# Performance work log

Measured on AMD Instinct MI355X. Metric: run time of the kernel, lower is better.

Reference implementation:

```python
import jax, jax.numpy as jnp
import numpy as np

H, VS, VT, S, T = 512, 32000, 32000, 256, 256
EPS = 1e-12


def _normalize(x):
    # torch.nn.functional.normalize over last dim, p=2, eps=1e-12
    n = jnp.sqrt(jnp.sum(x * x, axis=-1, keepdims=True))
    return x / jnp.maximum(n, EPS)


def setup_inputs() -> dict:
    key = jax.random.key(0)
    ks = jax.random.split(key, 16)
    std = 0.01
    return {
        'src_nums': jax.random.randint(ks[0], (S,), 0, VS, dtype=jnp.int32),
        'tgt_nums': jax.random.randint(ks[1], (T,), 0, VT, dtype=jnp.int32),
        'enc_emb_W': std * jax.random.normal(ks[2], (VS, H), jnp.float32),
        'enc_h0': std * jax.random.normal(ks[3], (H,), jnp.float32),
        'enc_W_hi': std * jax.random.normal(ks[4], (H, H), jnp.float32),
        'enc_W_hh': std * jax.random.normal(ks[5], (H, H), jnp.float32),
        'enc_b': std * jax.random.normal(ks[6], (H,), jnp.float32),
        'dec_emb_W': std * jax.random.normal(ks[7], (VT, H), jnp.float32),
        'dec_h0': std * jax.random.normal(ks[8], (H,), jnp.float32),
        'dec_W_hi': std * jax.random.normal(ks[9], (H, H), jnp.float32),
        'dec_W_hh': std * jax.random.normal(ks[10], (H, H), jnp.float32),
        'dec_b': std * jax.random.normal(ks[11], (H,), jnp.float32),
        'tnh_W': std * jax.random.normal(ks[12], (H, 2 * H), jnp.float32),
        'tnh_b': std * jax.random.normal(ks[13], (H,), jnp.float32),
        'out_W': std * jax.random.normal(ks[14], (VT, H), jnp.float32),
    }


def reference(src_nums, tgt_nums, enc_emb_W, enc_h0, enc_W_hi, enc_W_hh, enc_b,
              dec_emb_W, dec_h0, dec_W_hi, dec_W_hh, dec_b, tnh_W, tnh_b, out_W):
    # ---- Encoder: embed + normalize, then sequential RNN ----
    src_emb = _normalize(enc_emb_W[src_nums])  # [S, H]

    def enc_step(h, e):
        h2 = jnp.tanh(enc_W_hi @ e + enc_W_hh @ h + enc_b)
        return h2, h2

    _, hs = jax.lax.scan(enc_step, enc_h0, src_emb)
    h_seq = jnp.concatenate([enc_h0[None, :], hs], axis=0)  # [S+1, H]

    # ---- Decoder: per-step attention + output + teacher-forced input ----
    def dec_step(h, t):
        # Bahdanau-style dot attention over encoder states
        weights = jax.nn.softmax(h_seq @ h)        # [S+1]
        c = weights @ h_seq                         # [H]
        z = jnp.tanh(tnh_W @ jnp.concatenate([c, h]) + tnh_b)  # [H]
        logp = jax.nn.log_softmax(out_W @ z)        # [VT]
        nll = -logp[t]
        e = _normalize(dec_emb_W[t])                # [H]
        h2 = jnp.tanh(dec_W_hi @ e + dec_W_hh @ h + dec_b)
        return h2, nll

    _, nlls = jax.lax.scan(dec_step, dec_h0, tgt_nums)
    return jnp.mean(nlls)
```

## Files before the change

kernel.cpp:

```cpp
#include <hip/hip_runtime.h>

typedef _Float16 f16;
typedef _Float16 f16x2 __attribute__((ext_vector_type(2)));
typedef _Float16 half8 __attribute__((ext_vector_type(8)));
typedef float f32x4 __attribute__((ext_vector_type(4)));

#define Hh 512
#define TT 256
#define VTOT 32000
#define S4H 100.0f
#define NO_ELEMS 16384000L
#define NT_ELEMS 524288L

__device__ inline int dot8i4(int a, int b, int c) {
#if __has_builtin(__builtin_amdgcn_sdot8)
    return __builtin_amdgcn_sdot8(a, b, c, false);
#else
    int s = c;
#pragma unroll
    for (int i = 0; i < 8; ++i)
        s += ((a << (28 - 4 * i)) >> 28) * ((b << (28 - 4 * i)) >> 28);
    return s;
#endif
}

__device__ inline float tanh_fast(float x) {
    float ax = fabsf(x);
    float t = __expf(-2.f * ax);
    float th = (1.f - t) * __builtin_amdgcn_rcpf(1.f + t);
    return copysignf(th, x);
}

__device__ inline float block_sum(float v, float* red) {
#pragma unroll
    for (int o = 1; o < 64; o <<= 1) v += __shfl_xor(v, o);
    if ((threadIdx.x & 63) == 0) red[threadIdx.x >> 6] = v;
    __syncthreads();
    v = red[0] + red[1] + red[2] + red[3];
    __syncthreads();
    return v;
}

__device__ inline float block_max(float v, float* red) {
#pragma unroll
    for (int o = 1; o < 64; o <<= 1) v = fmaxf(v, __shfl_xor(v, o));
    if ((threadIdx.x & 63) == 0) red[threadIdx.x >> 6] = v;
    __syncthreads();
    v = fmaxf(fmaxf(red[0], red[1]), fmaxf(red[2], red[3]));
    __syncthreads();
    return v;
}

__global__ void __launch_bounds__(256) k_front(
    const int* __restrict__ src, const int* __restrict__ tgt,
    const float* __restrict__ encW, const float* __restrict__ decW,
    const float* __restrict__ eh0, const float* __restrict__ dh0,
    const float* __restrict__ encWhh, const float* __restrict__ decWhh,
    const float* __restrict__ eWhi, const float* __restrict__ eb,
    const float* __restrict__ dWhi, const float* __restrict__ db,
    float* __restrict__ P, float* __restrict__ h_seq, float* __restrict__ Hd,
    unsigned int* __restrict__ Wq, float* __restrict__ sWf,
    float* __restrict__ denom, float* __restrict__ ltgt) {
    const int b = blockIdx.x, tid = threadIdx.x;
    if (b >= 272) {
        const int c = b - 272;
        float2 v = ((const float2*)(c ? dh0 : eh0))[tid];
        if (c == 0) {
            ((float2*)h_seq)[tid] = v;
#pragma unroll
            for (int k = 0; k < 8; ++k) denom[k * 256 + tid] = 0.f;
        } else {
            ((float2*)Hd)[tid] = v;
            ltgt[tid] = 0.f;
        }
        return;
    }
    if (b >= 16) {
        const int bc = b - 16;
        const int R = bc * 4 + (tid >> 6);
        const int c = R >> 9, r = R & 511, j = tid & 63;
        const float* s = (c ? decWhh : encWhh) + (size_t)r * Hh + j * 8;
        float4 v0 = ((const float4*)s)[0];
        float4 v1 = ((const float4*)s)[1];
        float vv[8] = {v0.x, v0.y, v0.z, v0.w, v1.x, v1.y, v1.z, v1.w};
        float m = 0.f;
#pragma unroll
        for (int k = 0; k < 8; ++k) m = fmaxf(m, fabsf(vv[k]));
#pragma unroll
        for (int o = 1; o < 64; o <<= 1) m = fmaxf(m, __shfl_xor(m, o));
        m = fmaxf(m, 1e-30f);
        float qs = 7.f / m;
        unsigned int dw = 0;
#pragma unroll
        for (int k = 0; k < 8; ++k) {
            int q = (int)rintf(vv[k] * qs);
            dw |= ((unsigned int)(q & 0xF)) << (4 * k);
        }
        const int u = j >> 2, dwi = j & 3;
        Wq[((((size_t)(c * 16 + u)) * 512 + r) << 2) + dwi] = dw;
        if (j == 0) sWf[c * 512 + r] = m * (1.f / (7.f * S4H));
        return;
    }
    const int c = b >> 3;
    const int v0 = (b & 7) * 64;
    const float* Wv = c ? dWhi : eWhi;
    const float* bias = c ? db : eb;
    const float* Etab = c ? decW : encW;
    const int w = tid >> 6, l = tid & 63;
    const int l15 = l & 15, l4 = l >> 4;
    __shared__ __align__(16) f16 Wt[64][136];
    __shared__ __align__(16) f16 Zt[256][136];
    __shared__ float norms[256];
    __shared__ int idxs[256];
    idxs[tid] = c ? tgt[tid] : src[tid];
    __syncthreads();
    {
        const float4* er = (const float4*)(Etab + (size_t)idxs[tid] * Hh);
        float s = 0.f;
        for (int j = 0; j < Hh / 4; ++j) {
            float4 v = er[j];
            s += v.x * v.x + v.y * v.y + v.z * v.z + v.w * v.w;
        }
        norms[tid] = 1.f / fmaxf(sqrtf(s), 1e-12f);
    }
    __syncthreads();

    f32x4 acc[16];
#pragma unroll
    for (int tt = 0; tt < 16; ++tt) acc[tt] = (f32x4){0.f, 0.f, 0.f, 0.f};

    for (int kc = 0; kc < 4; ++kc) {
        const int k0 = kc * 128;
#pragma unroll
        for (int p = 0; p < 8; ++p) {
            int g = p * 256 + tid;
            int row = g >> 5, f4 = g & 31;
            float4 v = *((const float4*)(Wv + (size_t)(v0 + row) * Hh + k0 + f4 * 4));
            f16x2 lo = {(f16)v.x, (f16)v.y};
            f16x2 hi = {(f16)v.z, (f16)v.w};
            uint2 u;
            u.x = __builtin_bit_cast(unsigned, lo);
            u.y = __builtin_bit_cast(unsigned, hi);
            *((uint2*)&Wt[row][f4 * 4]) = u;
        }
#pragma unroll
        for (int p = 0; p < 16; ++p) {
            int g = p * 256 + tid;
            int row = g >> 4, u = g & 15;
            const float* rs = Etab + (size_t)idxs[row] * Hh + k0 + u * 8;
            float4 a0 = ((const float4*)rs)[0];
            float4 a1 = ((const float4*)rs)[1];
            float nm = norms[row];
            f16x2 p0 = {(f16)(a0.x * nm), (f16)(a0.y * nm)};
            f16x2 p1 = {(f16)(a0.z * nm), (f16)(a0.w * nm)};
            f16x2 p2 = {(f16)(a1.x * nm), (f16)(a1.y * nm)};
            f16x2 p3 = {(f16)(a1.z * nm), (f16)(a1.w * nm)};
            uint4 uu;
            uu.x = __builtin_bit_cast(unsigned, p0);
            uu.y = __builtin_bit_cast(unsigned, p1);
            uu.z = __builtin_bit_cast(unsigned, p2);
            uu.w = __builtin_bit_cast(unsigned, p3);
            *((uint4*)&Zt[row][u * 8]) = uu;
        }
        __syncthreads();
        half8 a[4];
#pragma unroll
        for (int ks = 0; ks < 4; ++ks)
            a[ks] = *((const half8*)&Wt[w * 16 + l15][ks * 32 + l4 * 8]);
#pragma unroll
        for (int tt = 0; tt < 16; ++tt) {
#pragma unroll
            for (int ks = 0; ks < 4; ++ks) {
                half8 bb = *((const half8*)&Zt[tt * 16 + l15][ks * 32 + l4 * 8]);
                acc[tt] = __builtin_amdgcn_mfma_f32_16x16x32_f16(a[ks], bb, acc[tt],
                                                                 0, 0, 0);
            }
        }
        __syncthreads();
    }
    const int ibase = v0 + w * 16 + l4 * 4;
    float b0 = bias[ibase], b1 = bias[ibase + 1];
    float b2 = bias[ibase + 2], b3 = bias[ibase + 3];
#pragma unroll
    for (int tt = 0; tt < 16; ++tt) {
        int t = tt * 16 + l15;
        float4 st;
        st.x = acc[tt][0] + b0;
        st.y = acc[tt][1] + b1;
        st.z = acc[tt][2] + b2;
        st.w = acc[tt][3] + b3;
        *((float4*)(P + ((size_t)c * TT + t) * Hh + ibase)) = st;
    }
}

__global__ void __launch_bounds__(512, 2) k_chain(
    const uint4* __restrict__ Wq, const float* __restrict__ sWf,
    const float* __restrict__ P, const float* __restrict__ eh0,
    const float* __restrict__ dh0, float* __restrict__ h_seq,
    float* __restrict__ Hd, const float* __restrict__ outW,
    const float* __restrict__ tnhW, f16* __restrict__ outWh,
    f16* __restrict__ tnhWh) {
    const int c = blockIdx.x, t = threadIdx.x;
    if (c >= 2) {
        const long nthreads = (long)(gridDim.x - 2) * 512;
        long g = (long)(c - 2) * 512 + t;
        const long N8 = (NO_ELEMS + NT_ELEMS) / 8;
        for (; g < N8; g += nthreads) {
            long e = g * 8;
            const float* s;
            f16* d;
            if (e < NO_ELEMS) {
                s = outW + e;
                d = outWh + e;
            } else {
                s = tnhW + (e - NO_ELEMS);
                d = tnhWh + (e - NO_ELEMS);
            }
            float4 v0 = ((const float4*)s)[0];
            float4 v1 = ((const float4*)s)[1];
            f16x2 p0 = {(f16)v0.x, (f16)v0.y};
            f16x2 p1 = {(f16)v0.z, (f16)v0.w};
            f16x2 p2 = {(f16)v1.x, (f16)v1.y};
            f16x2 p3 = {(f16)v1.z, (f16)v1.w};
            uint4 u;
            u.x = __builtin_bit_cast(unsigned, p0);
            u.y = __builtin_bit_cast(unsigned, p1);
            u.z = __builtin_bit_cast(unsigned, p2);
            u.w = __builtin_bit_cast(unsigned, p3);
            *((uint4*)d) = u;
        }
        return;
    }
    __shared__ __align__(16) int hq[2][64];

    uint4 wq[16];
#pragma unroll
    for (int u = 0; u < 16; ++u) wq[u] = Wq[(size_t)(c * 16 + u) * 512 + t];
#pragma unroll
    for (int u = 0; u < 16; ++u)
        asm volatile("" : "+v"(wq[u].x), "+v"(wq[u].y), "+v"(wq[u].z),
                          "+v"(wq[u].w));
    const float frow = sWf[c * 512 + t];

    {
        float hv = (c ? dh0 : eh0)[t];
        int q = (int)rintf(fminf(fmaxf(hv * S4H, -7.f), 7.f));
        int b1 = (q & 0xF) | ((__shfl_down(q, 1) & 0xF) << 4);
        int b2 = (b1 & 0xFF) | ((__shfl_down(b1, 2) & 0xFF) << 8);
        int b4 = (b2 & 0xFFFF) | (__shfl_down(b2, 4) << 16);
        if ((t & 7) == 0) hq[0][t >> 3] = b4;
    }
    __syncthreads();

    const float* Pc = P + (size_t)c * TT * Hh;
    float pv = Pc[t];

    for (int step = 0; step < 256; ++step) {
        float pvn;
        if (step < 255) pvn = Pc[(size_t)(step + 1) * Hh + t];
        const uint4* hp = (const uint4*)hq[step & 1];
        int a0 = 0, a1 = 0;
#pragma unroll
        for (int u = 0; u < 16; ++u) {
            uint4 hv = hp[u];
            uint4 w0 = wq[u];
            a0 = dot8i4((int)w0.x, (int)hv.x, a0);
            a1 = dot8i4((int)w0.y, (int)hv.y, a1);
            a0 = dot8i4((int)w0.z, (int)hv.z, a0);
            a1 = dot8i4((int)w0.w, (int)hv.w, a1);
        }
        float hnew = tanh_fast((float)(a0 + a1) * frow + pv);
        pv = pvn;
        if (c == 0)
            h_seq[(size_t)(step + 1) * Hh + t] = hnew;
        else if (step < 255)
            Hd[(size_t)(step + 1) * Hh + t] = hnew;
        int q = (int)rintf(fminf(fmaxf(hnew * S4H, -7.f), 7.f));
        int b1 = (q & 0xF) | ((__shfl_down(q, 1) & 0xF) << 4);
        int b2 = (b1 & 0xFF) | ((__shfl_down(b1, 2) & 0xFF) << 8);
        int b4 = (b2 & 0xFFFF) | (__shfl_down(b2, 4) << 16);
        if ((t & 7) == 0) hq[(step + 1) & 1][t >> 3] = b4;
        asm volatile("s_waitcnt lgkmcnt(0)\ns_barrier" ::: "memory");
    }
}

__global__ void __launch_bounds__(256) k_scores(const float* __restrict__ h_seq,
                                                const float* __restrict__ Hd,
                                                f16* __restrict__ CHh) {
    const int t0 = blockIdx.x * 4, tid = threadIdx.x;
    __shared__ float hs[4][Hh];
    __shared__ float wts[4][260];
    __shared__ float red[4];
#pragma unroll
    for (int q = 0; q < 4; ++q)
        ((float2*)hs[q])[tid] = ((const float2*)(Hd + (size_t)(t0 + q) * Hh))[tid];
    __syncthreads();
    float a[4] = {0.f, 0.f, 0.f, 0.f};
    {
        const float4* row = (const float4*)(h_seq + (size_t)tid * Hh);
        for (int j = 0; j < Hh / 4; ++j) {
            float4 v = row[j];
#pragma unroll
            for (int q = 0; q < 4; ++q) {
                a[q] += v.x * hs[q][4 * j] + v.y * hs[q][4 * j + 1] +
                        v.z * hs[q][4 * j + 2] + v.w * hs[q][4 * j + 3];
            }
        }
    }
    float sb[4] = {-3.0e38f, -3.0e38f, -3.0e38f, -3.0e38f};
    if (tid == 0) {
        const float4* row = (const float4*)(h_seq + (size_t)256 * Hh);
        float x[4] = {0.f, 0.f, 0.f, 0.f};
        for (int j = 0; j < Hh / 4; ++j) {
            float4 v = row[j];
#pragma unroll
            for (int q = 0; q < 4; ++q) {
                x[q] += v.x * hs[q][4 * j] + v.y * hs[q][4 * j + 1] +
                        v.z * hs[q][4 * j + 2] + v.w * hs[q][4 * j + 3];
            }
        }
#pragma unroll
        for (int q = 0; q < 4; ++q) sb[q] = x[q];
    }
#pragma unroll
    for (int q = 0; q < 4; ++q) {
        float m = block_max(fmaxf(a[q], sb[q]), red);
        float e = expf(a[q] - m);
        float ee = (tid == 0) ? expf(sb[q] - m) : 0.f;
        float tot = block_sum(e + ee, red);
        float inv = 1.f / tot;
        wts[q][tid] = e * inv;
        if (tid == 0) wts[q][256] = ee * inv;
    }
    __syncthreads();
    const float2* hs2 = (const float2*)h_seq;
    float2 cc[4];
#pragma unroll
    for (int q = 0; q < 4; ++q) cc[q] = (float2){0.f, 0.f};
    for (int s = 0; s < 257; ++s) {
        float2 v = hs2[(size_t)s * 256 + tid];
#pragma unroll
        for (int q = 0; q < 4; ++q) {
            float W = wts[q][s];
            cc[q].x += W * v.x;
            cc[q].y += W * v.y;
        }
    }
#pragma unroll
    for (int q = 0; q < 4; ++q) {
        f16* ch = CHh + (size_t)(t0 + q) * (2 * Hh);
        f16x2 o = {(f16)cc[q].x, (f16)cc[q].y};
        ((f16x2*)ch)[tid] = o;
        float2 hh = ((float2*)hs[q])[tid];
        f16x2 ho = {(f16)hh.x, (f16)hh.y};
        ((f16x2*)(ch + Hh))[tid] = ho;
    }
}

template <bool W16>
__global__ void __launch_bounds__(256) k_zmfma(const f16* __restrict__ CHh,
                                               const float* __restrict__ tnhW,
                                               const f16* __restrict__ tnhWh,
                                               const float* __restrict__ tnhb,
                                               f16* __restrict__ Zh) {
    const int v0 = blockIdx.x * 64, t0 = blockIdx.y * 128, tid = threadIdx.x;
    const int w = tid >> 6, l = tid & 63;
    const int l15 = l & 15, l4 = l >> 4;
    __shared__ __align__(16) f16 Wt[64][136];
    __shared__ __align__(16) f16 Zt[128][136];

    f32x4 acc[8];
#pragma unroll
    for (int tt = 0; tt < 8; ++tt) acc[tt] = (f32x4){0.f, 0.f, 0.f, 0.f};

    for (int kc = 0; kc < 8; ++kc) {
        const int k0 = kc * 128;
        if constexpr (W16) {
#pragma unroll
            for (int p = 0; p < 4; ++p) {
                int g = p * 256 + tid;
                int row = g >> 4, u = g & 15;
                *((uint4*)&Wt[row][u * 8]) =
                    *((const uint4*)(tnhWh + (size_t)(v0 + row) * 1024 + k0 + u * 8));
            }
        } else {
#pragma unroll
            for (int p = 0; p < 8; ++p) {
                int g = p * 256 + tid;
                int row = g >> 5, f4 = g & 31;
                float4 v =
                    *((const float4*)(tnhW + (size_t)(v0 + row) * 1024 + k0 + f4 * 4));
                f16x2 lo = {(f16)v.x, (f16)v.y};
                f16x2 hi = {(f16)v.z, (f16)v.w};
                uint2 u;
                u.x = __builtin_bit_cast(unsigned, lo);
                u.y = __builtin_bit_cast(unsigned, hi);
                *((uint2*)&Wt[row][f4 * 4]) = u;
            }
        }
#pragma unroll
        for (int p = 0; p < 8; ++p) {
            int g = p * 256 + tid;
            int row = g >> 4, u = g & 15;
            *((uint4*)&Zt[row][u * 8]) =
                *((const uint4*)(CHh + (size_t)(t0 + row) * 1024 + k0 + u * 8));
        }
        __syncthreads();
        half8 a[4];
#pragma unroll
        for (int ks = 0; ks < 4; ++ks)
            a[ks] = *((const half8*)&Wt[w * 16 + l15][ks * 32 + l4 * 8]);
#pragma unroll
        for (int tt = 0; tt < 8; ++tt) {
#pragma unroll
            for (int ks = 0; ks < 4; ++ks) {
                half8 bb = *((const half8*)&Zt[tt * 16 + l15][ks * 32 + l4 * 8]);
                acc[tt] = __builtin_amdgcn_mfma_f32_16x16x32_f16(a[ks], bb, acc[tt],
                                                                 0, 0, 0);
            }
        }
        __syncthreads();
    }
    const int ibase = v0 + w * 16 + l4 * 4;
    float b0 = tnhb[ibase], b1 = tnhb[ibase + 1];
    float b2 = tnhb[ibase + 2], b3 = tnhb[ibase + 3];
#pragma unroll
    for (int tt = 0; tt < 8; ++tt) {
        int t = t0 + tt * 16 + l15;
        f16x2 lo = {(f16)tanhf(acc[tt][0] + b0), (f16)tanhf(acc[tt][1] + b1)};
        f16x2 hi = {(f16)tanhf(acc[tt][2] + b2), (f16)tanhf(acc[tt][3] + b3)};
        uint2 u;
        u.x = __builtin_bit_cast(unsigned, lo);
        u.y = __builtin_bit_cast(unsigned, hi);
        *((uint2*)(Zh + (size_t)t * Hh + ibase)) = u;
    }
}

template <bool W16>
__global__ void __launch_bounds__(512) k_logits(const f16* __restrict__ Zh,
                                                const float* __restrict__ outW,
                                                const f16* __restrict__ outWh,
                                                const int* __restrict__ tgt,
                                                float* __restrict__ denom,
                                                float* __restrict__ ltgt) {
    const int v0 = blockIdx.x * 128, tid = threadIdx.x;
    const int w = tid >> 6, l = tid & 63;
    const int l15 = l & 15, l4 = l >> 4;
    __shared__ __align__(16) f16 Wt[128][136];
    __shared__ __align__(16) f16 Zt[256][136];
    __shared__ float tsum[8][256];
    __shared__ int tgs[256];
    if (tid < 256) tgs[tid] = tgt[tid];

    f32x4 acc[16];
#pragma unroll
    for (int tt = 0; tt < 16; ++tt) acc[tt] = (f32x4){0.f, 0.f, 0.f, 0.f};

    for (int kc = 0; kc < 4; ++kc) {
        const int k0 = kc * 128;
        if constexpr (W16) {
#pragma unroll
            for (int p = 0; p < 4; ++p) {
                int g = p * 512 + tid;
                int row = g >> 4, u = g & 15;
                *((uint4*)&Wt[row][u * 8]) =
                    *((const uint4*)(outWh + (size_t)(v0 + row) * Hh + k0 + u * 8));
            }
        } else {
#pragma unroll
            for (int p = 0; p < 8; ++p) {
                int g = p * 512 + tid;
                int row = g >> 5, f4 = g & 31;
                float4 v =
                    *((const float4*)(outW + (size_t)(v0 + row) * Hh + k0 + f4 * 4));
                f16x2 lo = {(f16)v.x, (f16)v.y};
                f16x2 hi = {(f16)v.z, (f16)v.w};
                uint2 u;
                u.x = __builtin_bit_cast(unsigned, lo);
                u.y = __builtin_bit_cast(unsigned, hi);
                *((uint2*)&Wt[row][f4 * 4]) = u;
            }
        }
#pragma unroll
        for (int p = 0; p < 8; ++p) {
            int g = p * 512 + tid;
            int row = g >> 4, u = g & 15;
            *((uint4*)&Zt[row][u * 8]) =
                *((const uint4*)(Zh + (size_t)row * Hh + k0 + u * 8));
        }
        __syncthreads();
        half8 a[4];
#pragma unroll
        for (int ks = 0; ks < 4; ++ks)
            a[ks] = *((const half8*)&Wt[w * 16 + l15][ks * 32 + l4 * 8]);
#pragma unroll
        for (int tt = 0; tt < 16; ++tt) {
#pragma unroll
            for (int ks = 0; ks < 4; ++ks) {
                half8 bb = *((const half8*)&Zt[tt * 16 + l15][ks * 32 + l4 * 8]);
                acc[tt] = __builtin_amdgcn_mfma_f32_16x16x32_f16(a[ks], bb, acc[tt],
                                                                 0, 0, 0);
            }
        }
        __syncthreads();
    }
    const int vbase = v0 + w * 16 + l4 * 4;
#pragma unroll
    for (int tt = 0; tt < 16; ++tt) {
        float e = __expf(acc[tt][0]) + __expf(acc[tt][1]) + __expf(acc[tt][2]) +
                  __expf(acc[tt][3]);
        e += __shfl_xor(e, 16);
        e += __shfl_xor(e, 32);
        if (l4 == 0) tsum[w][tt * 16 + l15] = e;
        int tglob = tt * 16 + l15;
        int rel = tgs[tglob] - vbase;
        if (rel >= 0 && rel < 4) {
            float val = (rel == 0) ? acc[tt][0]
                        : (rel == 1) ? acc[tt][1]
                        : (rel == 2) ? acc[tt][2]
                                     : acc[tt][3];
            ltgt[tglob] = val;
        }
    }
    __syncthreads();
    if (tid < 256) {
        float s = 0.f;
#pragma unroll
        for (int k = 0; k < 8; ++k) s += tsum[k][tid];
        atomicAdd(&denom[(blockIdx.x & 7) * 256 + tid], s);
    }
}

__global__ void k_final(const float* __restrict__ denom, const float* __restrict__ ltgt,
                        float* __restrict__ out) {
    const int t = threadIdx.x;
    float d = 0.f;
#pragma unroll
    for (int k = 0; k < 8; ++k) d += denom[k * 256 + t];
    float nll = logf(d) - ltgt[t];
    __shared__ float red[4];
    float v = nll;
#pragma unroll
    for (int o = 1; o < 64; o <<= 1) v += __shfl_xor(v, o);
    if ((t & 63) == 0) red[t >> 6] = v;
    __syncthreads();
    if (t == 0) out[0] = (red[0] + red[1] + red[2] + red[3]) * (1.f / 256.f);
}

extern "C" void kernel_launch(void* const* d_in, const int* in_sizes, int n_in,
                              void* d_out, int out_size, void* d_ws, size_t ws_size,
                              hipStream_t stream) {
    (void)in_sizes; (void)n_in; (void)out_size;
    const int* src = (const int*)d_in[0];
    const int* tgt = (const int*)d_in[1];
    const float* enc_emb = (const float*)d_in[2];
    const float* enc_h0 = (const float*)d_in[3];
    const float* enc_Whi = (const float*)d_in[4];
    const float* enc_Whh = (const float*)d_in[5];
    const float* enc_b = (const float*)d_in[6];
    const float* dec_emb = (const float*)d_in[7];
    const float* dec_h0 = (const float*)d_in[8];
    const float* dec_Whi = (const float*)d_in[9];
    const float* dec_Whh = (const float*)d_in[10];
    const float* dec_b = (const float*)d_in[11];
    const float* tnhW = (const float*)d_in[12];
    const float* tnhb = (const float*)d_in[13];
    const float* outW = (const float*)d_in[14];
    float* out = (float*)d_out;
    char* ws = (char*)d_ws;

    float* denom = (float*)ws;
    float* ltgt = (float*)(ws + 8192);
    size_t off = 16384;
    float* P = (float*)(ws + off);      off += (size_t)2 * TT * Hh * 4;
    float* h_seq = (float*)(ws + off);  off += (size_t)264 * Hh * 4;
    float* Hd = (float*)(ws + off);     off += (size_t)256 * Hh * 4;
    f16* CHh = (f16*)(ws + off);        off += (size_t)TT * 2 * Hh * 2;
    f16* Zh = (f16*)(ws + off);         off += (size_t)TT * Hh * 2;
    uint4* Wq = (uint4*)(ws + off);     off += (size_t)2 * Hh * Hh;
    float* sWf = (float*)(ws + off);    off += (size_t)2 * Hh * 4;
    f16* outWh = (f16*)(ws + off);      size_t off_big = off + NO_ELEMS * 2;
    f16* tnhWh = (f16*)(ws + off_big);  off_big += NT_ELEMS * 2;
    const bool big = ws_size >= off_big;

    k_front<<<274, 256, 0, stream>>>(src, tgt, enc_emb, dec_emb, enc_h0, dec_h0,
                                     enc_Whh, dec_Whh, enc_Whi, enc_b, dec_Whi,
                                     dec_b, P, h_seq, Hd, (unsigned int*)Wq, sWf,
                                     denom, ltgt);
    if (big) {
        k_chain<<<128, 512, 0, stream>>>(Wq, sWf, P, enc_h0, dec_h0, h_seq, Hd,
                                         outW, tnhW, outWh, tnhWh);
    } else {
        k_chain<<<2, 512, 0, stream>>>(Wq, sWf, P, enc_h0, dec_h0, h_seq, Hd,
                                       outW, tnhW, outWh, tnhWh);
    }
    k_scores<<<64, 256, 0, stream>>>(h_seq, Hd, CHh);
    if (big) {
        k_zmfma<true><<<dim3(8, 2), 256, 0, stream>>>(CHh, tnhW, tnhWh, tnhb, Zh);
        k_logits<true><<<250, 512, 0, stream>>>(Zh, outW, outWh, tgt, denom, ltgt);
    } else {
        k_zmfma<false><<<dim3(8, 2), 256, 0, stream>>>(CHh, tnhW, tnhWh, tnhb, Zh);
        k_logits<false><<<250, 512, 0, stream>>>(Zh, outW, outWh, tgt, denom, ltgt);
    }
    k_final<<<1, 256, 0, stream>>>(denom, ltgt, out);
}
```

Baseline: 302.5 us.

## Fuse pipeline into two persistent megakernels synchronized by global atomic counters

Replaces the chain of six launches (front, chain, scores, zmfma, logits, final) with a zeroing kernel plus two megakernels. Inside each one, blocks hand off work through release/acquire counters in global memory: the recurrence blocks spin until the projections and quantized weights are ready, the logits blocks wait for the tanh-projection blocks, and the last block to finish computes the final mean. The aim is to remove launch gaps and tail serialization between stages. The cost is spin-wait deadlock risk if the waiting blocks are not co-resident with the blocks they wait on, a bounded spin that silently gives up, and larger shared memory per block.

```diff
diff --git a/kernel.cpp b/kernel.cpp
--- a/kernel.cpp
+++ b/kernel.cpp
@@ -11,6 +11,7 @@
 #define S4H 100.0f
 #define NO_ELEMS 16384000L
 #define NT_ELEMS 524288L
+#define NFRONT 146
 
 __device__ inline int dot8i4(int a, int b, int c) {
 #if __has_builtin(__builtin_amdgcn_sdot8)
@@ -31,27 +32,54 @@
     return copysignf(th, x);
 }
 
-__device__ inline float block_sum(float v, float* red) {
+__device__ inline void rel_add(int* p) {
+    __hip_atomic_fetch_add(p, 1, __ATOMIC_RELEASE, __HIP_MEMORY_SCOPE_AGENT);
+}
+__device__ inline void acq_spin(int* p, int target) {
+    if (threadIdx.x == 0) {
+        int g = 0;
+        while (__hip_atomic_load(p, __ATOMIC_ACQUIRE, __HIP_MEMORY_SCOPE_AGENT) <
+               target) {
+            __builtin_amdgcn_s_sleep(2);
+            if (++g > (1 << 24)) break;
+        }
+    }
+    __syncthreads();
+}
+
+__device__ inline float bsum8(float v, float* red) {
 #pragma unroll
     for (int o = 1; o < 64; o <<= 1) v += __shfl_xor(v, o);
     if ((threadIdx.x & 63) == 0) red[threadIdx.x >> 6] = v;
     __syncthreads();
-    v = red[0] + red[1] + red[2] + red[3];
-    __syncthreads();
-    return v;
-}
-
-__device__ inline float block_max(float v, float* red) {
+    float s = 0.f;
+#pragma unroll
+    for (int k = 0; k < 8; ++k) s += red[k];
+    __syncthreads();
+    return s;
+}
+__device__ inline float bmax8(float v, float* red) {
 #pragma unroll
     for (int o = 1; o < 64; o <<= 1) v = fmaxf(v, __shfl_xor(v, o));
     if ((threadIdx.x & 63) == 0) red[threadIdx.x >> 6] = v;
     __syncthreads();
-    v = fmaxf(fmaxf(red[0], red[1]), fmaxf(red[2], red[3]));
-    __syncthreads();
-    return v;
-}
-
-__global__ void __launch_bounds__(256) k_front(
+    float m = red[0];
+#pragma unroll
+    for (int k = 1; k < 8; ++k) m = fmaxf(m, red[k]);
+    __syncthreads();
+    return m;
+}
+
+__global__ void k_zero(int* __restrict__ cnt, float* __restrict__ denom,
+                       float* __restrict__ ltgt) {
+    const int t = threadIdx.x;
+    if (t < 8) cnt[t] = 0;
+#pragma unroll
+    for (int k = 0; k < 8; ++k) denom[k * 256 + t] = 0.f;
+    ltgt[t] = 0.f;
+}
+
+__global__ void __launch_bounds__(512) k_mega1(
     const int* __restrict__ src, const int* __restrict__ tgt,
     const float* __restrict__ encW, const float* __restrict__ decW,
     const float* __restrict__ eh0, const float* __restrict__ dh0,
@@ -60,24 +88,171 @@
     const float* __restrict__ dWhi, const float* __restrict__ db,
     float* __restrict__ P, float* __restrict__ h_seq, float* __restrict__ Hd,
     unsigned int* __restrict__ Wq, float* __restrict__ sWf,
-    float* __restrict__ denom, float* __restrict__ ltgt) {
+    const float* __restrict__ outW, const float* __restrict__ tnhW,
+    f16* __restrict__ outWh, f16* __restrict__ tnhWh, f16* __restrict__ CHh,
+    int* __restrict__ cnt, int big) {
     const int b = blockIdx.x, tid = threadIdx.x;
-    if (b >= 272) {
-        const int c = b - 272;
-        float2 v = ((const float2*)(c ? dh0 : eh0))[tid];
-        if (c == 0) {
-            ((float2*)h_seq)[tid] = v;
-#pragma unroll
-            for (int k = 0; k < 8; ++k) denom[k * 256 + tid] = 0.f;
-        } else {
-            ((float2*)Hd)[tid] = v;
-            ltgt[tid] = 0.f;
-        }
+    __shared__ __align__(16) char SM[90112];
+
+    if (b < 2) {
+        const int c = b;
+        int* hq = (int*)SM;
+        acq_spin(cnt + 0, NFRONT);
+        const uint4* WqB = (const uint4*)Wq;
+        uint4 wq[16];
+#pragma unroll
+        for (int u = 0; u < 16; ++u) wq[u] = WqB[(size_t)(c * 16 + u) * 512 + tid];
+#pragma unroll
+        for (int u = 0; u < 16; ++u)
+            asm volatile("" : "+v"(wq[u].x), "+v"(wq[u].y), "+v"(wq[u].z),
+                              "+v"(wq[u].w));
+        const float frow = sWf[c * 512 + tid];
+        {
+            float hv = (c ? dh0 : eh0)[tid];
+            int q = (int)rintf(fminf(fmaxf(hv * S4H, -7.f), 7.f));
+            int b1 = (q & 0xF) | ((__shfl_down(q, 1) & 0xF) << 4);
+            int b2 = (b1 & 0xFF) | ((__shfl_down(b1, 2) & 0xFF) << 8);
+            int b4 = (b2 & 0xFFFF) | (__shfl_down(b2, 4) << 16);
+            if ((tid & 7) == 0) hq[tid >> 3] = b4;
+        }
+        __syncthreads();
+        const float* Pc = P + (size_t)c * TT * Hh;
+        float pv = Pc[tid];
+        for (int step = 0; step < 256; ++step) {
+            float pvn;
+            if (step < 255) pvn = Pc[(size_t)(step + 1) * Hh + tid];
+            const uint4* hp = (const uint4*)(hq + (step & 1) * 64);
+            int a0 = 0, a1 = 0;
+#pragma unroll
+            for (int u = 0; u < 16; ++u) {
+                uint4 hv = hp[u];
+                uint4 w0 = wq[u];
+                a0 = dot8i4((int)w0.x, (int)hv.x, a0);
+                a1 = dot8i4((int)w0.y, (int)hv.y, a1);
+                a0 = dot8i4((int)w0.z, (int)hv.z, a0);
+                a1 = dot8i4((int)w0.w, (int)hv.w, a1);
+            }
+            float hnew = tanh_fast((float)(a0 + a1) * frow + pv);
+            pv = pvn;
+            if (c == 0)
+                h_seq[(size_t)(step + 1) * Hh + tid] = hnew;
+            else if (step < 255)
+                Hd[(size_t)(step + 1) * Hh + tid] = hnew;
+            int q = (int)rintf(fminf(fmaxf(hnew * S4H, -7.f), 7.f));
+            int b1 = (q & 0xF) | ((__shfl_down(q, 1) & 0xF) << 4);
+            int b2 = (b1 & 0xFF) | ((__shfl_down(b1, 2) & 0xFF) << 8);
+            int b4 = (b2 & 0xFFFF) | (__shfl_down(b2, 4) << 16);
+            if ((tid & 7) == 0) hq[((step + 1) & 1) * 64 + (tid >> 3)] = b4;
+            asm volatile("s_waitcnt lgkmcnt(0)\ns_barrier" ::: "memory");
+        }
+        __syncthreads();
+        if (tid == 0) rel_add(cnt + 1);
         return;
     }
-    if (b >= 16) {
-        const int bc = b - 16;
-        const int R = bc * 4 + (tid >> 6);
+
+    if (b < 18) {
+        const int bb = b - 2;
+        const int c = bb >> 3;
+        const int v0 = (bb & 7) * 64;
+        const float* Wv = c ? dWhi : eWhi;
+        const float* bias = c ? db : eb;
+        const float* Etab = c ? decW : encW;
+        f16* Wt = (f16*)SM;
+        f16* Zt = (f16*)(SM + 17408);
+        float* norms = (float*)(SM + 87040);
+        int* idxs = (int*)(SM + 88064);
+        const int w = tid >> 6, l = tid & 63;
+        const int l15 = l & 15, l4 = l >> 4;
+        if (tid < 256) idxs[tid] = c ? tgt[tid] : src[tid];
+        __syncthreads();
+        if (tid < 256) {
+            const float4* er = (const float4*)(Etab + (size_t)idxs[tid] * Hh);
+            float s = 0.f;
+            for (int j = 0; j < Hh / 4; ++j) {
+                float4 v = er[j];
+                s += v.x * v.x + v.y * v.y + v.z * v.z + v.w * v.w;
+            }
+            norms[tid] = 1.f / fmaxf(sqrtf(s), 1e-12f);
+        }
+        __syncthreads();
+        f32x4 acc[16];
+#pragma unroll
+        for (int tt = 0; tt < 16; ++tt) acc[tt] = (f32x4){0.f, 0.f, 0.f, 0.f};
+        for (int kc = 0; kc < 4; ++kc) {
+            const int k0 = kc * 128;
+#pragma unroll
+            for (int p = 0; p < 4; ++p) {
+                int g = p * 512 + tid;
+                int row = g >> 5, f4 = g & 31;
+                float4 v =
+                    *((const float4*)(Wv + (size_t)(v0 + row) * Hh + k0 + f4 * 4));
+                f16x2 lo = {(f16)v.x, (f16)v.y};
+                f16x2 hi = {(f16)v.z, (f16)v.w};
+                uint2 u;
+                u.x = __builtin_bit_cast(unsigned, lo);
+                u.y = __builtin_bit_cast(unsigned, hi);
+                *((uint2*)&Wt[row * 136 + f4 * 4]) = u;
+            }
+#pragma unroll
+            for (int p = 0; p < 8; ++p) {
+                int g = p * 512 + tid;
+                int row = g >> 4, u = g & 15;
+                const float* rs = Etab + (size_t)idxs[row] * Hh + k0 + u * 8;
+                float4 a0 = ((const float4*)rs)[0];
+                float4 a1 = ((const float4*)rs)[1];
+                float nm = norms[row];
+                f16x2 p0 = {(f16)(a0.x * nm), (f16)(a0.y * nm)};
+                f16x2 p1 = {(f16)(a0.z * nm), (f16)(a0.w * nm)};
+                f16x2 p2 = {(f16)(a1.x * nm), (f16)(a1.y * nm)};
+                f16x2 p3 = {(f16)(a1.z * nm), (f16)(a1.w * nm)};
+                uint4 uu;
+                uu.x = __builtin_bit_cast(unsigned, p0);
+                uu.y = __builtin_bit_cast(unsigned, p1);
+                uu.z = __builtin_bit_cast(unsigned, p2);
+                uu.w = __builtin_bit_cast(unsigned, p3);
+                *((uint4*)&Zt[row * 136 + u * 8]) = uu;
+            }
+            __syncthreads();
+            if (w < 4) {
+                half8 a[4];
+#pragma unroll
+                for (int ks = 0; ks < 4; ++ks)
+                    a[ks] = *((const half8*)&Wt[(w * 16 + l15) * 136 + ks * 32 + l4 * 8]);
+#pragma unroll
+                for (int tt = 0; tt < 16; ++tt) {
+#pragma unroll
+                    for (int ks = 0; ks < 4; ++ks) {
+                        half8 bb2 = *((const half8*)&Zt[(tt * 16 + l15) * 136 +
+                                                        ks * 32 + l4 * 8]);
+                        acc[tt] = __builtin_amdgcn_mfma_f32_16x16x32_f16(
+                            a[ks], bb2, acc[tt], 0, 0, 0);
+                    }
+                }
+            }
+            __syncthreads();
+        }
+        if (w < 4) {
+            const int ibase = v0 + w * 16 + l4 * 4;
+            float b0 = bias[ibase], b1 = bias[ibase + 1];
+            float b2 = bias[ibase + 2], b3 = bias[ibase + 3];
+#pragma unroll
+            for (int tt = 0; tt < 16; ++tt) {
+                int t = tt * 16 + l15;
+                float4 st;
+                st.x = acc[tt][0] + b0;
+                st.y = acc[tt][1] + b1;
+                st.z = acc[tt][2] + b2;
+                st.w = acc[tt][3] + b3;
+                *((float4*)(P + ((size_t)c * TT + t) * Hh + ibase)) = st;
+            }
+        }
+        __syncthreads();
+        if (tid == 0) rel_add(cnt + 0);
+        return;
+    }
+
+    if (b < 146) {
+        const int R = (b - 18) * 8 + (tid >> 6);
         const int c = R >> 9, r = R & 511, j = tid & 63;
         const float* s = (c ? decWhh : encWhh) + (size_t)r * Hh + j * 8;
         float4 v0 = ((const float4*)s)[0];
@@ -99,111 +274,28 @@
         const int u = j >> 2, dwi = j & 3;
         Wq[((((size_t)(c * 16 + u)) * 512 + r) << 2) + dwi] = dw;
         if (j == 0) sWf[c * 512 + r] = m * (1.f / (7.f * S4H));
+        __syncthreads();
+        if (tid == 0) rel_add(cnt + 0);
         return;
     }
-    const int c = b >> 3;
-    const int v0 = (b & 7) * 64;
-    const float* Wv = c ? dWhi : eWhi;
-    const float* bias = c ? db : eb;
-    const float* Etab = c ? decW : encW;
-    const int w = tid >> 6, l = tid & 63;
-    const int l15 = l & 15, l4 = l >> 4;
-    __shared__ __align__(16) f16 Wt[64][136];
-    __shared__ __align__(16) f16 Zt[256][136];
-    __shared__ float norms[256];
-    __shared__ int idxs[256];
-    idxs[tid] = c ? tgt[tid] : src[tid];
-    __syncthreads();
-    {
-        const float4* er = (const float4*)(Etab + (size_t)idxs[tid] * Hh);
-        float s = 0.f;
-        for (int j = 0; j < Hh / 4; ++j) {
-            float4 v = er[j];
-            s += v.x * v.x + v.y * v.y + v.z * v.z + v.w * v.w;
-        }
-        norms[tid] = 1.f / fmaxf(sqrtf(s), 1e-12f);
-    }
-    __syncthreads();
-
-    f32x4 acc[16];
-#pragma unroll
-    for (int tt = 0; tt < 16; ++tt) acc[tt] = (f32x4){0.f, 0.f, 0.f, 0.f};
-
-    for (int kc = 0; kc < 4; ++kc) {
-        const int k0 = kc * 128;
-#pragma unroll
-        for (int p = 0; p < 8; ++p) {
-            int g = p * 256 + tid;
-            int row = g >> 5, f4 = g & 31;
-            float4 v = *((const float4*)(Wv + (size_t)(v0 + row) * Hh + k0 + f4 * 4));
-            f16x2 lo = {(f16)v.x, (f16)v.y};
-            f16x2 hi = {(f16)v.z, (f16)v.w};
-            uint2 u;
-            u.x = __builtin_bit_cast(unsigned, lo);
-            u.y = __builtin_bit_cast(unsigned, hi);
-            *((uint2*)&Wt[row][f4 * 4]) = u;
-        }
-#pragma unroll
-        for (int p = 0; p < 16; ++p) {
-            int g = p * 256 + tid;
-            int row = g >> 4, u = g & 15;
-            const float* rs = Etab + (size_t)idxs[row] * Hh + k0 + u * 8;
-            float4 a0 = ((const float4*)rs)[0];
-            float4 a1 = ((const float4*)rs)[1];
-            float nm = norms[row];
-            f16x2 p0 = {(f16)(a0.x * nm), (f16)(a0.y * nm)};
-            f16x2 p1 = {(f16)(a0.z * nm), (f16)(a0.w * nm)};
-            f16x2 p2 = {(f16)(a1.x * nm), (f16)(a1.y * nm)};
-            f16x2 p3 = {(f16)(a1.z * nm), (f16)(a1.w * nm)};
-            uint4 uu;
-            uu.x = __builtin_bit_cast(unsigned, p0);
-            uu.y = __builtin_bit_cast(unsigned, p1);
-            uu.z = __builtin_bit_cast(unsigned, p2);
-            uu.w = __builtin_bit_cast(unsigned, p3);
-            *((uint4*)&Zt[row][u * 8]) = uu;
-        }
-        __syncthreads();
-        half8 a[4];
-#pragma unroll
-        for (int ks = 0; ks < 4; ++ks)
-            a[ks] = *((const half8*)&Wt[w * 16 + l15][ks * 32 + l4 * 8]);
-#pragma unroll
-        for (int tt = 0; tt < 16; ++tt) {
-#pragma unroll
-            for (int ks = 0; ks < 4; ++ks) {
-                half8 bb = *((const half8*)&Zt[tt * 16 + l15][ks * 32 + l4 * 8]);
-                acc[tt] = __builtin_amdgcn_mfma_f32_16x16x32_f16(a[ks], bb, acc[tt],
-                                                                 0, 0, 0);
-            }
-        }
-        __syncthreads();
-    }
-    const int ibase = v0 + w * 16 + l4 * 4;
-    float b0 = bias[ibase], b1 = bias[ibase + 1];
-    float b2 = bias[ibase + 2], b3 = bias[ibase + 3];
-#pragma unroll
-    for (int tt = 0; tt < 16; ++tt) {
-        int t = tt * 16 + l15;
-        float4 st;
-        st.x = acc[tt][0] + b0;
-        st.y = acc[tt][1] + b1;
-        st.z = acc[tt][2] + b2;
-        st.w = acc[tt][3] + b3;
-        *((float4*)(P + ((size_t)c * TT + t) * Hh + ibase)) = st;
-    }
-}
-
-__global__ void __launch_bounds__(512, 2) k_chain(
-    const uint4* __restrict__ Wq, const float* __restrict__ sWf,
-    const float* __restrict__ P, const float* __restrict__ eh0,
-    const float* __restrict__ dh0, float* __restrict__ h_seq,
-    float* __restrict__ Hd, const float* __restrict__ outW,
-    const float* __restrict__ tnhW, f16* __restrict__ outWh,
-    f16* __restrict__ tnhWh) {
-    const int c = blockIdx.x, t = threadIdx.x;
-    if (c >= 2) {
-        const long nthreads = (long)(gridDim.x - 2) * 512;
-        long g = (long)(c - 2) * 512 + t;
+
+    if (b < 148) {
+        const int c = b - 146;
+        if (tid < 256) {
+            float2 v = ((const float2*)(c ? dh0 : eh0))[tid];
+            if (c == 0)
+                ((float2*)h_seq)[tid] = v;
+            else
+                ((float2*)Hd)[tid] = v;
+        }
+        __syncthreads();
+        if (tid == 0) rel_add(cnt + 0);
+        return;
+    }
+
+    if (big) {
+        const long nthreads = 64L * 512L;
+        long g = (long)(b - 148) * 512 + tid;
         const long N8 = (NO_ELEMS + NT_ELEMS) / 8;
         for (; g < N8; g += nthreads) {
             long e = g * 8;
@@ -229,233 +321,155 @@
             u.w = __builtin_bit_cast(unsigned, p3);
             *((uint4*)d) = u;
         }
-        return;
-    }
-    __shared__ __align__(16) int hq[2][64];
-
-    uint4 wq[16];
-#pragma unroll
-    for (int u = 0; u < 16; ++u) wq[u] = Wq[(size_t)(c * 16 + u) * 512 + t];
-#pragma unroll
-    for (int u = 0; u < 16; ++u)
-        asm volatile("" : "+v"(wq[u].x), "+v"(wq[u].y), "+v"(wq[u].z),
-                          "+v"(wq[u].w));
-    const float frow = sWf[c * 512 + t];
-
+    }
+    acq_spin(cnt + 1, 2);
     {
-        float hv = (c ? dh0 : eh0)[t];
-        int q = (int)rintf(fminf(fmaxf(hv * S4H, -7.f), 7.f));
-        int b1 = (q & 0xF) | ((__shfl_down(q, 1) & 0xF) << 4);
-        int b2 = (b1 & 0xFF) | ((__shfl_down(b1, 2) & 0xFF) << 8);
-        int b4 = (b2 & 0xFFFF) | (__shfl_down(b2, 4) << 16);
-        if ((t & 7) == 0) hq[0][t >> 3] = b4;
-    }
-    __syncthreads();
-
-    const float* Pc = P + (size_t)c * TT * Hh;
-    float pv = Pc[t];
-
-    for (int step = 0; step < 256; ++step) {
-        float pvn;
-        if (step < 255) pvn = Pc[(size_t)(step + 1) * Hh + t];
-        const uint4* hp = (const uint4*)hq[step & 1];
-        int a0 = 0, a1 = 0;
-#pragma unroll
-        for (int u = 0; u < 16; ++u) {
-            uint4 hv = hp[u];
-            uint4 w0 = wq[u];
-            a0 = dot8i4((int)w0.x, (int)hv.x, a0);
-            a1 = dot8i4((int)w0.y, (int)hv.y, a1);
-            a0 = dot8i4((int)w0.z, (int)hv.z, a0);
-            a1 = dot8i4((int)w0.w, (int)hv.w, a1);
-        }
-        float hnew = tanh_fast((float)(a0 + a1) * frow + pv);
-        pv = pvn;
-        if (c == 0)
-            h_seq[(size_t)(step + 1) * Hh + t] = hnew;
-        else if (step < 255)
-            Hd[(size_t)(step + 1) * Hh + t] = hnew;
-        int q = (int)rintf(fminf(fmaxf(hnew * S4H, -7.f), 7.f));
-        int b1 = (q & 0xF) | ((__shfl_down(q, 1) & 0xF) << 4);
-        int b2 = (b1 & 0xFF) | ((__shfl_down(b1, 2) & 0xFF) << 8);
-        int b4 = (b2 & 0xFFFF) | (__shfl_down(b2, 4) << 16);
-        if ((t & 7) == 0) hq[(step + 1) & 1][t >> 3] = b4;
-        asm volatile("s_waitcnt lgkmcnt(0)\ns_barrier" ::: "memory");
-    }
-}
-
-__global__ void __launch_bounds__(256) k_scores(const float* __restrict__ h_seq,
-                                                const float* __restrict__ Hd,
-                                                f16* __restrict__ CHh) {
-    const int t0 = blockIdx.x * 4, tid = threadIdx.x;
-    __shared__ float hs[4][Hh];
-    __shared__ float wts[4][260];
-    __shared__ float red[4];
-#pragma unroll
-    for (int q = 0; q < 4; ++q)
-        ((float2*)hs[q])[tid] = ((const float2*)(Hd + (size_t)(t0 + q) * Hh))[tid];
-    __syncthreads();
-    float a[4] = {0.f, 0.f, 0.f, 0.f};
-    {
-        const float4* row = (const float4*)(h_seq + (size_t)tid * Hh);
-        for (int j = 0; j < Hh / 4; ++j) {
-            float4 v = row[j];
-#pragma unroll
-            for (int q = 0; q < 4; ++q) {
-                a[q] += v.x * hs[q][4 * j] + v.y * hs[q][4 * j + 1] +
-                        v.z * hs[q][4 * j + 2] + v.w * hs[q][4 * j + 3];
-            }
-        }
-    }
-    float sb[4] = {-3.0e38f, -3.0e38f, -3.0e38f, -3.0e38f};
-    if (tid == 0) {
-        const float4* row = (const float4*)(h_seq + (size_t)256 * Hh);
-        float x[4] = {0.f, 0.f, 0.f, 0.f};
-        for (int j = 0; j < Hh / 4; ++j) {
-            float4 v = row[j];
-#pragma unroll
-            for (int q = 0; q < 4; ++q) {
-                x[q] += v.x * hs[q][4 * j] + v.y * hs[q][4 * j + 1] +
-                        v.z * hs[q][4 * j + 2] + v.w * hs[q][4 * j + 3];
-            }
-        }
-#pragma unroll
-        for (int q = 0; q < 4; ++q) sb[q] = x[q];
-    }
-#pragma unroll
-    for (int q = 0; q < 4; ++q) {
-        float m = block_max(fmaxf(a[q], sb[q]), red);
-        float e = expf(a[q] - m);
-        float ee = (tid == 0) ? expf(sb[q] - m) : 0.f;
-        float tot = block_sum(e + ee, red);
-        float inv = 1.f / tot;
-        wts[q][tid] = e * inv;
-        if (tid == 0) wts[q][256] = ee * inv;
-    }
-    __syncthreads();
-    const float2* hs2 = (const float2*)h_seq;
-    float2 cc[4];
-#pragma unroll
-    for (int q = 0; q < 4; ++q) cc[q] = (float2){0.f, 0.f};
-    for (int s = 0; s < 257; ++s) {
-        float2 v = hs2[(size_t)s * 256 + tid];
+        float* hs = (float*)SM;
+        float* wts = hs + 4 * 512;
+        float* red = wts + 4 * 260;
+        const int t0 = (b - 148) * 4;
+#pragma unroll
+        for (int q = 0; q < 4; ++q)
+            hs[q * 512 + tid] = Hd[(size_t)(t0 + q) * Hh + tid];
+        __syncthreads();
+        const bool act = (tid <= 256);
+        float a[4] = {-3.0e38f, -3.0e38f, -3.0e38f, -3.0e38f};
+        if (act) {
+            const float4* row = (const float4*)(h_seq + (size_t)tid * Hh);
+            float x[4] = {0.f, 0.f, 0.f, 0.f};
+            for (int j = 0; j < Hh / 4; ++j) {
+                float4 v = row[j];
+#pragma unroll
+                for (int q = 0; q < 4; ++q) {
+                    x[q] += v.x * hs[q * 512 + 4 * j] + v.y * hs[q * 512 + 4 * j + 1] +
+                            v.z * hs[q * 512 + 4 * j + 2] +
+                            v.w * hs[q * 512 + 4 * j + 3];
+                }
+            }
+#pragma unroll
+            for (int q = 0; q < 4; ++q) a[q] = x[q];
+        }
 #pragma unroll
         for (int q = 0; q < 4; ++q) {
-            float W = wts[q][s];
-            cc[q].x += W * v.x;
-            cc[q].y += W * v.y;
-        }
-    }
-#pragma unroll
-    for (int q = 0; q < 4; ++q) {
-        f16* ch = CHh + (size_t)(t0 + q) * (2 * Hh);
-        f16x2 o = {(f16)cc[q].x, (f16)cc[q].y};
-        ((f16x2*)ch)[tid] = o;
-        float2 hh = ((float2*)hs[q])[tid];
-        f16x2 ho = {(f16)hh.x, (f16)hh.y};
-        ((f16x2*)(ch + Hh))[tid] = ho;
+            float m = bmax8(a[q], red);
+            float e = act ? __expf(a[q] - m) : 0.f;
+            float tot = bsum8(e, red);
+            if (act) wts[q * 260 + tid] = e * __builtin_amdgcn_rcpf(tot);
+        }
+        __syncthreads();
+        float c4[4] = {0.f, 0.f, 0.f, 0.f};
+        for (int s = 0; s < 257; ++s) {
+            float v = h_seq[(size_t)s * Hh + tid];
+#pragma unroll
+            for (int q = 0; q < 4; ++q) c4[q] += wts[q * 260 + s] * v;
+        }
+#pragma unroll
+        for (int q = 0; q < 4; ++q) {
+            f16* ch = CHh + (size_t)(t0 + q) * (2 * Hh);
+            ch[tid] = (f16)c4[q];
+            ch[Hh + tid] = (f16)hs[q * 512 + tid];
+        }
     }
 }
 
 template <bool W16>
-__global__ void __launch_bounds__(256) k_zmfma(const f16* __restrict__ CHh,
-                                               const float* __restrict__ tnhW,
-                                               const f16* __restrict__ tnhWh,
-                                               const float* __restrict__ tnhb,
-                                               f16* __restrict__ Zh) {
-    const int v0 = blockIdx.x * 64, t0 = blockIdx.y * 128, tid = threadIdx.x;
-    const int w = tid >> 6, l = tid & 63;
-    const int l15 = l & 15, l4 = l >> 4;
-    __shared__ __align__(16) f16 Wt[64][136];
-    __shared__ __align__(16) f16 Zt[128][136];
-
-    f32x4 acc[8];
-#pragma unroll
-    for (int tt = 0; tt < 8; ++tt) acc[tt] = (f32x4){0.f, 0.f, 0.f, 0.f};
-
-    for (int kc = 0; kc < 8; ++kc) {
-        const int k0 = kc * 128;
-        if constexpr (W16) {
-#pragma unroll
-            for (int p = 0; p < 4; ++p) {
-                int g = p * 256 + tid;
-                int row = g >> 4, u = g & 15;
-                *((uint4*)&Wt[row][u * 8]) =
-                    *((const uint4*)(tnhWh + (size_t)(v0 + row) * 1024 + k0 + u * 8));
-            }
-        } else {
-#pragma unroll
-            for (int p = 0; p < 8; ++p) {
-                int g = p * 256 + tid;
-                int row = g >> 5, f4 = g & 31;
-                float4 v =
-                    *((const float4*)(tnhW + (size_t)(v0 + row) * 1024 + k0 + f4 * 4));
-                f16x2 lo = {(f16)v.x, (f16)v.y};
-                f16x2 hi = {(f16)v.z, (f16)v.w};
-                uint2 u;
-                u.x = __builtin_bit_cast(unsigned, lo);
-                u.y = __builtin_bit_cast(unsigned, hi);
-                *((uint2*)&Wt[row][f4 * 4]) = u;
-            }
-        }
-#pragma unroll
-        for (int p = 0; p < 8; ++p) {
-            int g = p * 256 + tid;
-            int row = g >> 4, u = g & 15;
-            *((uint4*)&Zt[row][u * 8]) =
-                *((const uint4*)(CHh + (size_t)(t0 + row) * 1024 + k0 + u * 8));
-        }
-        __syncthreads();
-        half8 a[4];
-#pragma unroll
-        for (int ks = 0; ks < 4; ++ks)
-            a[ks] = *((const half8*)&Wt[w * 16 + l15][ks * 32 + l4 * 8]);
-#pragma unroll
-        for (int tt = 0; tt < 8; ++tt) {
-#pragma unroll
-            for (int ks = 0; ks < 4; ++ks) {
-                half8 bb = *((const half8*)&Zt[tt * 16 + l15][ks * 32 + l4 * 8]);
-                acc[tt] = __builtin_amdgcn_mfma_f32_16x16x32_f16(a[ks], bb, acc[tt],
-                                                                 0, 0, 0);
-            }
-        }
-        __syncthreads();
-    }
-    const int ibase = v0 + w * 16 + l4 * 4;
-    float b0 = tnhb[ibase], b1 = tnhb[ibase + 1];
-    float b2 = tnhb[ibase + 2], b3 = tnhb[ibase + 3];
-#pragma unroll
-    for (int tt = 0; tt < 8; ++tt) {
-        int t = t0 + tt * 16 + l15;
-        f16x2 lo = {(f16)tanhf(acc[tt][0] + b0), (f16)tanhf(acc[tt][1] + b1)};
-        f16x2 hi = {(f16)tanhf(acc[tt][2] + b2), (f16)tanhf(acc[tt][3] + b3)};
-        uint2 u;
-        u.x = __builtin_bit_cast(unsigned, lo);
-        u.y = __builtin_bit_cast(unsigned, hi);
-        *((uint2*)(Zh + (size_t)t * Hh + ibase)) = u;
-    }
-}
-
-template <bool W16>
-__global__ void __launch_bounds__(512) k_logits(const f16* __restrict__ Zh,
-                                                const float* __restrict__ outW,
-                                                const f16* __restrict__ outWh,
-                                                const int* __restrict__ tgt,
-                                                float* __restrict__ denom,
-                                                float* __restrict__ ltgt) {
-    const int v0 = blockIdx.x * 128, tid = threadIdx.x;
+__global__ void __launch_bounds__(512) k_mega2(
+    const f16* __restrict__ CHh, const float* __restrict__ tnhW,
+    const f16* __restrict__ tnhWh, const float* __restrict__ tnhb,
+    f16* __restrict__ Zh, const float* __restrict__ outW,
+    const f16* __restrict__ outWh, const int* __restrict__ tgt,
+    float* __restrict__ denom, float* __restrict__ ltgt, float* __restrict__ out,
+    int* __restrict__ cnt) {
+    const int b = blockIdx.x, tid = threadIdx.x;
     const int w = tid >> 6, l = tid & 63;
     const int l15 = l & 15, l4 = l >> 4;
     __shared__ __align__(16) f16 Wt[128][136];
     __shared__ __align__(16) f16 Zt[256][136];
     __shared__ float tsum[8][256];
     __shared__ int tgs[256];
+    __shared__ int lastf;
+
+    if (b < 16) {
+        const int v0 = (b & 7) * 64, t0 = (b >> 3) * 128;
+        f32x4 acc[8];
+#pragma unroll
+        for (int tt = 0; tt < 8; ++tt) acc[tt] = (f32x4){0.f, 0.f, 0.f, 0.f};
+        for (int kc = 0; kc < 8; ++kc) {
+            const int k0 = kc * 128;
+            if constexpr (W16) {
+#pragma unroll
+                for (int p = 0; p < 2; ++p) {
+                    int g = p * 512 + tid;
+                    int row = g >> 4, u = g & 15;
+                    *((uint4*)&Wt[row][u * 8]) = *(
+                        (const uint4*)(tnhWh + (size_t)(v0 + row) * 1024 + k0 + u * 8));
+                }
+            } else {
+#pragma unroll
+                for (int p = 0; p < 4; ++p) {
+                    int g = p * 512 + tid;
+                    int row = g >> 5, f4 = g & 31;
+                    float4 v = *((const float4*)(tnhW + (size_t)(v0 + row) * 1024 +
+                                                 k0 + f4 * 4));
+                    f16x2 lo = {(f16)v.x, (f16)v.y};
+                    f16x2 hi = {(f16)v.z, (f16)v.w};
+                    uint2 u;
+                    u.x = __builtin_bit_cast(unsigned, lo);
+                    u.y = __builtin_bit_cast(unsigned, hi);
+                    *((uint2*)&Wt[row][f4 * 4]) = u;
+                }
+            }
+#pragma unroll
+            for (int p = 0; p < 4; ++p) {
+                int g = p * 512 + tid;
+                int row = g >> 4, u = g & 15;
+                *((uint4*)&Zt[row][u * 8]) =
+                    *((const uint4*)(CHh + (size_t)(t0 + row) * 1024 + k0 + u * 8));
+            }
+            __syncthreads();
+            if (w < 4) {
+                half8 a[4];
+#pragma unroll
+                for (int ks = 0; ks < 4; ++ks)
+                    a[ks] = *((const half8*)&Wt[w * 16 + l15][ks * 32 + l4 * 8]);
+#pragma unroll
+                for (int tt = 0; tt < 8; ++tt) {
+#pragma unroll
+                    for (int ks = 0; ks < 4; ++ks) {
+                        half8 bb = *((const half8*)&Zt[tt * 16 + l15][ks * 32 + l4 * 8]);
+                        acc[tt] = __builtin_amdgcn_mfma_f32_16x16x32_f16(a[ks], bb,
+                                                                         acc[tt], 0, 0, 0);
+                    }
+                }
+            }
+            __syncthreads();
+        }
+        if (w < 4) {
+            const int ibase = v0 + w * 16 + l4 * 4;
+            float b0 = tnhb[ibase], b1 = tnhb[ibase + 1];
+            float b2 = tnhb[ibase + 2], b3 = tnhb[ibase + 3];
+#pragma unroll
+            for (int tt = 0; tt < 8; ++tt) {
+                int t = t0 + tt * 16 + l15;
+                f16x2 lo = {(f16)tanhf(acc[tt][0] + b0), (f16)tanhf(acc[tt][1] + b1)};
+                f16x2 hi = {(f16)tanhf(acc[tt][2] + b2), (f16)tanhf(acc[tt][3] + b3)};
+                uint2 u;
+                u.x = __builtin_bit_cast(unsigned, lo);
+                u.y = __builtin_bit_cast(unsigned, hi);
+                *((uint2*)(Zh + (size_t)t * Hh + ibase)) = u;
+            }
+        }
+        __syncthreads();
+        if (tid == 0) rel_add(cnt + 2);
+    }
+    acq_spin(cnt + 2, 16);
+
+    const int v0 = b * 128;
     if (tid < 256) tgs[tid] = tgt[tid];
-
+    __syncthreads();
     f32x4 acc[16];
 #pragma unroll
     for (int tt = 0; tt < 16; ++tt) acc[tt] = (f32x4){0.f, 0.f, 0.f, 0.f};
-
     for (int kc = 0; kc < 4; ++kc) {
         const int k0 = kc * 128;
         if constexpr (W16) {
@@ -527,24 +541,26 @@
         float s = 0.f;
 #pragma unroll
         for (int k = 0; k < 8; ++k) s += tsum[k][tid];
-        atomicAdd(&denom[(blockIdx.x & 7) * 256 + tid], s);
-    }
-}
-
-__global__ void k_final(const float* __restrict__ denom, const float* __restrict__ ltgt,
-                        float* __restrict__ out) {
-    const int t = threadIdx.x;
-    float d = 0.f;
-#pragma unroll
-    for (int k = 0; k < 8; ++k) d += denom[k * 256 + t];
-    float nll = logf(d) - ltgt[t];
-    __shared__ float red[4];
-    float v = nll;
-#pragma unroll
-    for (int o = 1; o < 64; o <<= 1) v += __shfl_xor(v, o);
-    if ((t & 63) == 0) red[t >> 6] = v;
-    __syncthreads();
-    if (t == 0) out[0] = (red[0] + red[1] + red[2] + red[3]) * (1.f / 256.f);
+        atomicAdd(&denom[(b & 7) * 256 + tid], s);
+    }
+    __syncthreads();
+    if (tid == 0) {
+        int old = __hip_atomic_fetch_add(cnt + 3, 1, __ATOMIC_ACQ_REL,
+                                         __HIP_MEMORY_SCOPE_AGENT);
+        lastf = (old == (int)gridDim.x - 1) ? 1 : 0;
+    }
+    __syncthreads();
+    if (lastf) {
+        float v = 0.f;
+        if (tid < 256) {
+            float d = 0.f;
+#pragma unroll
+            for (int k = 0; k < 8; ++k) d += denom[k * 256 + tid];
+            v = logf(d) - ltgt[tid];
+        }
+        float tot = bsum8(v, (float*)tsum);
+        if (tid == 0) out[0] = tot * (1.f / 256.f);
+    }
 }
 
 extern "C" void kernel_launch(void* const* d_in, const int* in_sizes, int n_in,
@@ -571,6 +587,7 @@
 
     float* denom = (float*)ws;
     float* ltgt = (float*)(ws + 8192);
+    int* cnt = (int*)(ws + 12288);
     size_t off = 16384;
     float* P = (float*)(ws + off);      off += (size_t)2 * TT * Hh * 4;
     float* h_seq = (float*)(ws + off);  off += (size_t)264 * Hh * 4;
@@ -583,24 +600,17 @@
     f16* tnhWh = (f16*)(ws + off_big);  off_big += NT_ELEMS * 2;
     const bool big = ws_size >= off_big;
 
-    k_front<<<274, 256, 0, stream>>>(src, tgt, enc_emb, dec_emb, enc_h0, dec_h0,
+    k_zero<<<1, 256, 0, stream>>>(cnt, denom, ltgt);
+    k_mega1<<<212, 512, 0, stream>>>(src, tgt, enc_emb, dec_emb, enc_h0, dec_h0,
                                      enc_Whh, dec_Whh, enc_Whi, enc_b, dec_Whi,
                                      dec_b, P, h_seq, Hd, (unsigned int*)Wq, sWf,
-                                     denom, ltgt);
+                                     outW, tnhW, outWh, tnhWh, CHh, cnt,
+                                     big ? 1 : 0);
     if (big) {
-        k_chain<<<128, 512, 0, stream>>>(Wq, sWf, P, enc_h0, dec_h0, h_seq, Hd,
-                                         outW, tnhW, outWh, tnhWh);
+        k_mega2<true><<<250, 512, 0, stream>>>(CHh, tnhW, tnhWh, tnhb, Zh, outW,
+                                               outWh, tgt, denom, ltgt, out, cnt);
     } else {
-        k_chain<<<2, 512, 0, stream>>>(Wq, sWf, P, enc_h0, dec_h0, h_seq, Hd,
-                                       outW, tnhW, outWh, tnhWh);
-    }
-    k_scores<<<64, 256, 0, stream>>>(h_seq, Hd, CHh);
-    if (big) {
-        k_zmfma<true><<<dim3(8, 2), 256, 0, stream>>>(CHh, tnhW, tnhWh, tnhb, Zh);
-        k_logits<true><<<250, 512, 0, stream>>>(Zh, outW, outWh, tgt, denom, ltgt);
-    } else {
-        k_zmfma<false><<<dim3(8, 2), 256, 0, stream>>>(CHh, tnhW, tnhWh, tnhb, Zh);
-        k_logits<false><<<250, 512, 0, stream>>>(Zh, outW, outWh, tgt, denom, ltgt);
-    }
-    k_final<<<1, 256, 0, stream>>>(denom, ltgt, out);
-}
+        k_mega2<false><<<250, 512, 0, stream>>>(CHh, tnhW, tnhWh, tnhb, Zh, outW,
+                                                outWh, tgt, denom, ltgt, out, cnt);
+    }
+}
```

Measured after the change: 327.8 us. +8.4%, slower.
